# Kernel tuning notes

Hardware: AMD Instinct MI355X
Metric: run time of the kernel (lower is better)

## Reference

```python
import jax, jax.numpy as jnp
import numpy as np

N_LAYER = 4
N_HEAD = 12
D_MODEL = 768
SEQ_LEN = 2048
VOCAB = 50257
BATCH = 2


def _sinusoid_pe(seq_len, d_model):
    pos = np.arange(seq_len, dtype=np.float32)[:, None]
    div = np.exp(np.arange(0, d_model, 2, dtype=np.float32) * (-np.log(10000.0) / d_model))
    pe = np.zeros((seq_len, d_model), dtype=np.float32)
    pe[:, 0::2] = np.sin(pos * div)
    pe[:, 1::2] = np.cos(pos * div)
    return jnp.asarray(pe[None])  # [1, C, D]


def setup_inputs() -> dict:
    key = jax.random.key(0)
    ks = jax.random.split(key, 12)
    s = 0.02
    return {
        "features": jax.random.randint(ks[0], (BATCH, SEQ_LEN), 0, VOCAB),
        "targets": jax.random.randint(ks[1], (BATCH, SEQ_LEN), 0, VOCAB),
        "tok_embed": jax.random.normal(ks[2], (VOCAB, D_MODEL), jnp.float32) * s,
        "pos_emb": _sinusoid_pe(SEQ_LEN, D_MODEL),
        "ln1_w": jnp.ones((N_LAYER, D_MODEL), jnp.float32),
        "ln1_b": jnp.zeros((N_LAYER, D_MODEL), jnp.float32),
        "attn_w": jax.random.normal(ks[3], (N_LAYER, D_MODEL, 3 * D_MODEL), jnp.float32) * s,
        "attn_b": jnp.zeros((N_LAYER, 3 * D_MODEL), jnp.float32),
        "proj_w": jax.random.normal(ks[4], (N_LAYER, D_MODEL, D_MODEL), jnp.float32) * s,
        "proj_b": jnp.zeros((N_LAYER, D_MODEL), jnp.float32),
        "ln2_w": jnp.ones((N_LAYER, D_MODEL), jnp.float32),
        "ln2_b": jnp.zeros((N_LAYER, D_MODEL), jnp.float32),
        "ffn_w1": jax.random.normal(ks[5], (N_LAYER, D_MODEL, 4 * D_MODEL), jnp.float32) * s,
        "ffn_b1": jnp.zeros((N_LAYER, 4 * D_MODEL), jnp.float32),
        "ffn_w2": jax.random.normal(ks[6], (N_LAYER, 4 * D_MODEL, D_MODEL), jnp.float32) * s,
        "ffn_b2": jnp.zeros((N_LAYER, D_MODEL), jnp.float32),
        "lnf_w": jnp.ones((D_MODEL,), jnp.float32),
        "lnf_b": jnp.zeros((D_MODEL,), jnp.float32),
        "final_w": jax.random.normal(ks[7], (D_MODEL, VOCAB), jnp.float32) * s,
    }


def _layernorm(x, w, b, eps=1e-5):
    mu = jnp.mean(x, axis=-1, keepdims=True)
    var = jnp.var(x, axis=-1, keepdims=True)
    return (x - mu) * jax.lax.rsqrt(var + eps) * w + b


def _attention(x, wqkv, bqkv, wo, bo):
    B, C, E = x.shape
    dh = E // N_HEAD
    qkv = x @ wqkv + bqkv  # [B, C, 3E]
    q, k, v = jnp.split(qkv, 3, axis=-1)
    q = q.reshape(B, C, N_HEAD, dh)
    k = k.reshape(B, C, N_HEAD, dh)
    v = v.reshape(B, C, N_HEAD, dh)
    att = jnp.einsum("bqhd,bkhd->bhqk", q, k) / jnp.sqrt(jnp.float32(dh))
    causal = jnp.tril(jnp.ones((C, C), bool))
    att = jnp.where(causal, att, -jnp.inf)
    att = jax.nn.softmax(att, axis=-1)
    y = jnp.einsum("bhqk,bkhd->bqhd", att, v).reshape(B, C, E)
    return y @ wo + bo


def reference(features, targets, tok_embed, pos_emb, ln1_w, ln1_b, attn_w, attn_b,
              proj_w, proj_b, ln2_w, ln2_b, ffn_w1, ffn_b1, ffn_w2, ffn_b2,
              lnf_w, lnf_b, final_w):
    C = features.shape[1]
    x = tok_embed[features] + pos_emb[:, :C]
    for l in range(N_LAYER):
        h = _layernorm(x, ln1_w[l], ln1_b[l])
        x = x + _attention(h, attn_w[l], attn_b[l], proj_w[l], proj_b[l])
        h = _layernorm(x, ln2_w[l], ln2_b[l])
        h = jax.nn.gelu(h @ ffn_w1[l] + ffn_b1[l], approximate=False) @ ffn_w2[l] + ffn_b2[l]
        x = x + h
    x = _layernorm(x, lnf_w, lnf_b)
    logits = x @ final_w  # [B, C, V]
    logp = jax.nn.log_softmax(logits, axis=-1)
    tgt = targets.reshape(-1)
    valid = tgt != -1
    tgt_safe = jnp.where(valid, tgt, 0)
    nll = -jnp.take_along_axis(logp.reshape(-1, logits.shape[-1]), tgt_safe[:, None], axis=1)[:, 0]
    loss = jnp.sum(jnp.where(valid, nll, 0.0)) / jnp.maximum(jnp.sum(valid), 1)
    return logits, loss
```

## Files before the change

kernel.cpp:

```cpp
#include <hip/hip_runtime.h>
#include <math.h>

#define N_LAYER 4
#define N_HEAD  12
#define D_MODEL 768
#define SEQ     2048
#define VOCAB   50257
#define BATCH   2
#define MROWS   (BATCH*SEQ)

typedef __bf16 bf16;
typedef __bf16 bf16x8 __attribute__((ext_vector_type(8)));
typedef float  f32x4  __attribute__((ext_vector_type(4)));
typedef short  short8v __attribute__((ext_vector_type(8)));

__device__ __forceinline__ void gload16(const bf16* g, const bf16* l) {
    __builtin_amdgcn_global_load_lds(
        (const __attribute__((address_space(1))) void*)g,
        (__attribute__((address_space(3))) void*)l,
        16, 0, 0);
}

__global__ __launch_bounds__(256) void embed_kernel(
    const int* __restrict__ feat, const float* __restrict__ tok,
    const float* __restrict__ pos, float* __restrict__ x)
{
    int row = blockIdx.x;
    int cpos = row & (SEQ - 1);
    int tid = feat[row];
    const float* te = tok + (size_t)tid * D_MODEL;
    const float* pe = pos + (size_t)cpos * D_MODEL;
    float* xr = x + (size_t)row * D_MODEL;
    for (int c = threadIdx.x; c < D_MODEL; c += 256)
        xr[c] = te[c] + pe[c];
}

__global__ __launch_bounds__(256) void ln_kernel(
    const float* __restrict__ x, const float* __restrict__ w,
    const float* __restrict__ b, bf16* __restrict__ out)
{
    int row = blockIdx.x;
    const float* xr = x + (size_t)row * D_MODEL;
    float lv[3];
    float s = 0.f, ss = 0.f;
#pragma unroll
    for (int i = 0; i < 3; i++) {
        float v = xr[threadIdx.x + i * 256];
        lv[i] = v; s += v; ss += v * v;
    }
#pragma unroll
    for (int o = 32; o; o >>= 1) { s += __shfl_down(s, o, 64); ss += __shfl_down(ss, o, 64); }
    __shared__ float red[8];
    int wid = threadIdx.x >> 6;
    if ((threadIdx.x & 63) == 0) { red[wid] = s; red[wid + 4] = ss; }
    __syncthreads();
    s  = red[0] + red[1] + red[2] + red[3];
    ss = red[4] + red[5] + red[6] + red[7];
    float mu  = s * (1.f / D_MODEL);
    float var = ss * (1.f / D_MODEL) - mu * mu;
    float rs  = rsqrtf(var + 1e-5f);
#pragma unroll
    for (int i = 0; i < 3; i++) {
        int c = threadIdx.x + i * 256;
        out[(size_t)row * D_MODEL + c] = (bf16)((lv[i] - mu) * rs * w[c] + b[c]);
    }
}

__global__ __launch_bounds__(256) void transpose_conv_kernel(
    const float* __restrict__ W, bf16* __restrict__ Wt, int K, int N)
{
    int l = blockIdx.z;
    const float* Wl = W + (size_t)l * K * N;
    bf16* Wtl = Wt + (size_t)l * K * N;
    __shared__ float tile[32][33];
    int k0 = blockIdx.y * 32, n0 = blockIdx.x * 32;
    for (int idx = threadIdx.x; idx < 1024; idx += 256) {
        int i = idx >> 5, j = idx & 31;
        int n = n0 + j;
        tile[i][j] = (n < N) ? Wl[(size_t)(k0 + i) * N + n] : 0.f;
    }
    __syncthreads();
    for (int idx = threadIdx.x; idx < 1024; idx += 256) {
        int j = idx >> 5, i = idx & 31;
        int n = n0 + j;
        if (n < N) Wtl[(size_t)n * K + k0 + i] = (bf16)tile[i][j];
    }
}

__global__ __launch_bounds__(256) void vtrans_kernel(
    const bf16* __restrict__ qkv, bf16* __restrict__ vT)
{
    int j0 = blockIdx.x * 64, h = blockIdx.y, b = blockIdx.z;
    __shared__ bf16 t[64][72];
    const bf16* src = qkv + ((size_t)b * SEQ + j0) * (3 * D_MODEL) + 2 * D_MODEL + h * 64;
    int tid = threadIdx.x;
#pragma unroll
    for (int i = 0; i < 2; i++) {
        int c = tid + i * 256;
        int j = c >> 3, d8 = (c & 7) * 8;
        *(short8v*)&t[j][d8] = *(const short8v*)&src[(size_t)j * (3 * D_MODEL) + d8];
    }
    __syncthreads();
    bf16* dst = vT + ((size_t)(b * N_HEAD + h) * 64) * SEQ;
#pragma unroll
    for (int i = 0; i < 2; i++) {
        int c = tid + i * 256;
        int d = c >> 3, j8 = (c & 7) * 8;
        bf16 tmp[8];
#pragma unroll
        for (int e = 0; e < 8; e++) tmp[e] = t[j8 + e][d];
        *(short8v*)&dst[(size_t)d * SEQ + j0 + j8] = *(const short8v*)tmp;
    }
}

template<bool BIAS, bool GELU_, int OUTM, bool SWZ, bool LSE>
__global__ __launch_bounds__(256) void gemm_kernel(
    const bf16* __restrict__ A, const bf16* __restrict__ Bt,
    const float* __restrict__ bias, void* __restrict__ Cout,
    float* __restrict__ rowsum,
    int M, int N, int K)
{
    __shared__ __align__(16) bf16 As[128 * 32];
    __shared__ __align__(16) bf16 Bs[128 * 32];
    int tid = threadIdx.x;
    int lane = tid & 63, wid = tid >> 6;

    int nbx = gridDim.x;
    int bid = blockIdx.y * nbx + blockIdx.x;
    if (SWZ) {
        int nwg = nbx * gridDim.y;
        int q = nwg >> 3, r = nwg & 7;
        int xcd = bid & 7, loc = bid >> 3;
        bid = (xcd < r ? xcd * (q + 1) : r * (q + 1) + (xcd - r) * q) + loc;
    }
    int row0 = (bid % nbx) * 128;
    int col0 = (bid / nbx) * 128;

    int wr = (wid >> 1) * 64, wc = (wid & 1) * 64;

    int srow = wid * 16 + (lane >> 2);
    int selem = (lane & 3) * 8;
    const bf16* Ab0 = A + (size_t)(row0 + srow) * K + selem;
    const bf16* Ab1 = Ab0 + (size_t)64 * K;
    int bn0 = col0 + srow;      if (bn0 >= N) bn0 = N - 1;
    int bn1 = col0 + srow + 64; if (bn1 >= N) bn1 = N - 1;
    const bf16* Bb0 = Bt + (size_t)bn0 * K + selem;
    const bf16* Bb1 = Bt + (size_t)bn1 * K + selem;
    bf16* ldsA0 = As + wid * 512;
    bf16* ldsA1 = As + (wid + 4) * 512;
    bf16* ldsB0 = Bs + wid * 512;
    bf16* ldsB1 = Bs + (wid + 4) * 512;

    f32x4 acc[4][4] = {};
    int fr = lane & 15, fg8 = (lane >> 4) * 8;

    for (int k0 = 0; k0 < K; k0 += 32) {
        if (k0) __syncthreads();
        gload16(Ab0 + k0, ldsA0);
        gload16(Ab1 + k0, ldsA1);
        gload16(Bb0 + k0, ldsB0);
        gload16(Bb1 + k0, ldsB1);
        __syncthreads();

        bf16x8 af[4], bfr[4];
#pragma unroll
        for (int m = 0; m < 4; m++) af[m] = *(const bf16x8*)&As[(wr + m * 16 + fr) * 32 + fg8];
#pragma unroll
        for (int n = 0; n < 4; n++) bfr[n] = *(const bf16x8*)&Bs[(wc + n * 16 + fr) * 32 + fg8];
#pragma unroll
        for (int m = 0; m < 4; m++)
#pragma unroll
            for (int n = 0; n < 4; n++)
                acc[m][n] = __builtin_amdgcn_mfma_f32_16x16x32_bf16(af[m], bfr[n], acc[m][n], 0, 0, 0);
    }

    int g = lane >> 4;
    float lsum[4][4];
#pragma unroll
    for (int m = 0; m < 4; m++)
#pragma unroll
        for (int r = 0; r < 4; r++) lsum[m][r] = 0.f;

#pragma unroll
    for (int m = 0; m < 4; m++) {
#pragma unroll
        for (int n = 0; n < 4; n++) {
            int col = col0 + wc + n * 16 + fr;
            bool ok = (col < N);
            float bv = (BIAS && ok) ? bias[col] : 0.f;
#pragma unroll
            for (int r = 0; r < 4; r++) {
                int row = row0 + wr + m * 16 + g * 4 + r;
                float v = acc[m][n][r] + bv;
                if (GELU_) v = 0.5f * v * (1.f + erff(v * 0.70710678118f));
                if (ok) {
                    if (OUTM == 0)      ((float*)Cout)[(size_t)row * N + col] = v;
                    else if (OUTM == 1) ((bf16*)Cout)[(size_t)row * N + col] = (bf16)v;
                    else                ((float*)Cout)[(size_t)row * N + col] += v;
                }
                if (LSE) lsum[m][r] += ok ? __expf(v) : 0.f;
            }
        }
    }

    if (LSE) {
#pragma unroll
        for (int m = 0; m < 4; m++)
#pragma unroll
            for (int r = 0; r < 4; r++) {
                float s = lsum[m][r];
#pragma unroll
                for (int o = 1; o < 16; o <<= 1) s += __shfl_xor(s, o, 64);
                lsum[m][r] = s;
            }
        if (fr == 0) {
#pragma unroll
            for (int m = 0; m < 4; m++)
#pragma unroll
                for (int r = 0; r < 4; r++)
                    atomicAdd(&rowsum[row0 + wr + m * 16 + g * 4 + r], lsum[m][r]);
        }
    }
}

__global__ __launch_bounds__(256) void attn_kernel(
    const bf16* __restrict__ qkv, const bf16* __restrict__ vT, bf16* __restrict__ y)
{
    int qt = blockIdx.x, h = blockIdx.y, b = blockIdx.z;
    const size_t rs = 3 * D_MODEL;
    int tid = threadIdx.x, lane = tid & 63, wid = tid >> 6;
    int fr = lane & 15, g = lane >> 4;
    int wq = qt * 64 + wid * 16;

    const bf16* qb = qkv + (size_t)b * SEQ * rs + h * 64;
    const bf16* kb = qb + D_MODEL;
    const bf16* vb = vT + ((size_t)(b * N_HEAD + h) * 64) * SEQ;

    __shared__ bf16 Ps[4][16][72];

    bf16x8 aq[2];
#pragma unroll
    for (int kk = 0; kk < 2; kk++)
        aq[kk] = *(const bf16x8*)&qb[(size_t)(wq + fr) * rs + kk * 32 + g * 8];

    f32x4 acco[4] = {};
    float mrow[4], lrow[4];
#pragma unroll
    for (int r = 0; r < 4; r++) { mrow[r] = -1e30f; lrow[r] = 0.f; }

    int jmax = qt * 64;
    for (int j0 = 0; j0 <= jmax; j0 += 64) {
        f32x4 accs[4] = {};
#pragma unroll
        for (int n = 0; n < 4; n++)
#pragma unroll
            for (int kk = 0; kk < 2; kk++) {
                bf16x8 bk = *(const bf16x8*)&kb[(size_t)(j0 + n * 16 + fr) * rs + kk * 32 + g * 8];
                accs[n] = __builtin_amdgcn_mfma_f32_16x16x32_bf16(aq[kk], bk, accs[n], 0, 0, 0);
            }

        bool diag = (j0 == jmax);
#pragma unroll
        for (int n = 0; n < 4; n++) {
            int jc = j0 + n * 16 + fr;
#pragma unroll
            for (int r = 0; r < 4; r++) {
                float sv = accs[n][r] * 0.125f;
                if (diag) { int irow = wq + g * 4 + r; if (jc > irow) sv = -1e30f; }
                accs[n][r] = sv;
            }
        }

        float pscale[4];
#pragma unroll
        for (int r = 0; r < 4; r++) {
            float pm = fmaxf(fmaxf(accs[0][r], accs[1][r]), fmaxf(accs[2][r], accs[3][r]));
#pragma unroll
            for (int o = 1; o < 16; o <<= 1) pm = fmaxf(pm, __shfl_xor(pm, o, 64));
            float mnew = fmaxf(mrow[r], pm);
            float corr = __expf(mrow[r] - mnew);
            mrow[r] = mnew;
            float ls = 0.f;
#pragma unroll
            for (int n = 0; n < 4; n++) {
                float p = __expf(accs[n][r] - mnew);
                accs[n][r] = p; ls += p;
            }
#pragma unroll
            for (int o = 1; o < 16; o <<= 1) ls += __shfl_xor(ls, o, 64);
            lrow[r] = lrow[r] * corr + ls;
            pscale[r] = corr;
        }
#pragma unroll
        for (int n = 0; n < 4; n++)
#pragma unroll
            for (int r = 0; r < 4; r++) acco[n][r] *= pscale[r];

#pragma unroll
        for (int n = 0; n < 4; n++)
#pragma unroll
            for (int r = 0; r < 4; r++)
                Ps[wid][g * 4 + r][n * 16 + fr] = (bf16)accs[n][r];

        bf16x8 ap[2];
#pragma unroll
        for (int kk = 0; kk < 2; kk++)
            ap[kk] = *(const bf16x8*)&Ps[wid][fr][kk * 32 + g * 8];
#pragma unroll
        for (int kk = 0; kk < 2; kk++)
#pragma unroll
            for (int n = 0; n < 4; n++) {
                bf16x8 bv = *(const bf16x8*)&vb[(size_t)(n * 16 + fr) * SEQ + j0 + kk * 32 + g * 8];
                acco[n] = __builtin_amdgcn_mfma_f32_16x16x32_bf16(ap[kk], bv, acco[n], 0, 0, 0);
            }
    }

    bf16* yb = y + (size_t)b * SEQ * D_MODEL + h * 64;
#pragma unroll
    for (int n = 0; n < 4; n++)
#pragma unroll
        for (int r = 0; r < 4; r++) {
            int row = wq + g * 4 + r;
            yb[(size_t)row * D_MODEL + n * 16 + fr] = (bf16)(acco[n][r] / lrow[r]);
        }
}

__global__ __launch_bounds__(256) void loss_nll_kernel(
    const float* __restrict__ logits, const float* __restrict__ rowsum,
    const int* __restrict__ tgt, float* __restrict__ accum)
{
    int row = blockIdx.x * 256 + threadIdx.x;
    if (row >= MROWS) return;
    int t = tgt[row];
    if (t >= 0) {
        float nll = logf(rowsum[row]) - logits[(size_t)row * VOCAB + t];
        atomicAdd(accum, nll);
        atomicAdd(accum + 1, 1.f);
    }
}

__global__ void loss_final_kernel(const float* __restrict__ accum, float* __restrict__ out)
{
    out[0] = accum[0] / fmaxf(accum[1], 1.f);
}

extern "C" void kernel_launch(void* const* d_in, const int* in_sizes, int n_in,
                              void* d_out, int out_size, void* d_ws, size_t ws_size,
                              hipStream_t stream)
{
    const int*   feat  = (const int*)d_in[0];
    const int*   tgt   = (const int*)d_in[1];
    const float* tok   = (const float*)d_in[2];
    const float* pos   = (const float*)d_in[3];
    const float* ln1w  = (const float*)d_in[4];
    const float* ln1b  = (const float*)d_in[5];
    const float* attnw = (const float*)d_in[6];
    const float* attnb = (const float*)d_in[7];
    const float* projw = (const float*)d_in[8];
    const float* projb = (const float*)d_in[9];
    const float* ln2w  = (const float*)d_in[10];
    const float* ln2b  = (const float*)d_in[11];
    const float* fw1   = (const float*)d_in[12];
    const float* fb1   = (const float*)d_in[13];
    const float* fw2   = (const float*)d_in[14];
    const float* fb2   = (const float*)d_in[15];
    const float* lnfw  = (const float*)d_in[16];
    const float* lnfb  = (const float*)d_in[17];
    const float* finw  = (const float*)d_in[18];

    char* ws = (char*)d_ws;
    size_t off = 0;
    auto alloc = [&](size_t bytes) -> void* {
        void* p = ws + off; off += (bytes + 255) & ~(size_t)255; return p;
    };
    float* x     = (float*)alloc((size_t)MROWS * D_MODEL * 4);
    bf16*  h     = (bf16*) alloc((size_t)MROWS * D_MODEL * 2);
    bf16*  big   = (bf16*) alloc((size_t)MROWS * 4 * D_MODEL * 2);
    bf16*  ybuf  = (bf16*) alloc((size_t)MROWS * D_MODEL * 2);
    bf16*  vT    = (bf16*) alloc((size_t)BATCH * N_HEAD * 64 * SEQ * 2);
    bf16*  awt   = (bf16*) alloc((size_t)N_LAYER * 3 * D_MODEL * D_MODEL * 2);
    bf16*  pwt   = (bf16*) alloc((size_t)N_LAYER * D_MODEL * D_MODEL * 2);
    bf16*  f1wt  = (bf16*) alloc((size_t)N_LAYER * 4 * D_MODEL * D_MODEL * 2);
    bf16*  f2wt  = (bf16*) alloc((size_t)N_LAYER * 4 * D_MODEL * D_MODEL * 2);
    bf16*  fwt   = (bf16*) alloc((size_t)VOCAB * D_MODEL * 2);
    float* rowsum= (float*)alloc((size_t)MROWS * 4);
    float* accum = (float*)alloc(256);

    float* logits = (float*)d_out;
    float* lossp  = (float*)d_out + (size_t)MROWS * VOCAB;

    dim3 blk(256);
    transpose_conv_kernel<<<dim3(3 * D_MODEL / 32, D_MODEL / 32, N_LAYER), blk, 0, stream>>>(attnw, awt, D_MODEL, 3 * D_MODEL);
    transpose_conv_kernel<<<dim3(D_MODEL / 32, D_MODEL / 32, N_LAYER), blk, 0, stream>>>(projw, pwt, D_MODEL, D_MODEL);
    transpose_conv_kernel<<<dim3(4 * D_MODEL / 32, D_MODEL / 32, N_LAYER), blk, 0, stream>>>(fw1, f1wt, D_MODEL, 4 * D_MODEL);
    transpose_conv_kernel<<<dim3(D_MODEL / 32, 4 * D_MODEL / 32, N_LAYER), blk, 0, stream>>>(fw2, f2wt, 4 * D_MODEL, D_MODEL);
    transpose_conv_kernel<<<dim3((VOCAB + 31) / 32, D_MODEL / 32, 1), blk, 0, stream>>>(finw, fwt, D_MODEL, VOCAB);

    embed_kernel<<<MROWS, blk, 0, stream>>>(feat, tok, pos, x);

    for (int l = 0; l < N_LAYER; l++) {
        ln_kernel<<<MROWS, blk, 0, stream>>>(x, ln1w + l * D_MODEL, ln1b + l * D_MODEL, h);
        gemm_kernel<true, false, 1, false, false><<<dim3(MROWS / 128, (3 * D_MODEL) / 128), blk, 0, stream>>>(
            h, awt + (size_t)l * 3 * D_MODEL * D_MODEL, attnb + l * 3 * D_MODEL, big, nullptr,
            MROWS, 3 * D_MODEL, D_MODEL);
        vtrans_kernel<<<dim3(SEQ / 64, N_HEAD, BATCH), blk, 0, stream>>>(big, vT);
        attn_kernel<<<dim3(SEQ / 64, N_HEAD, BATCH), blk, 0, stream>>>(big, vT, ybuf);
        gemm_kernel<true, false, 2, false, false><<<dim3(MROWS / 128, D_MODEL / 128), blk, 0, stream>>>(
            ybuf, pwt + (size_t)l * D_MODEL * D_MODEL, projb + l * D_MODEL, x, nullptr,
            MROWS, D_MODEL, D_MODEL);
        ln_kernel<<<MROWS, blk, 0, stream>>>(x, ln2w + l * D_MODEL, ln2b + l * D_MODEL, h);
        gemm_kernel<true, true, 1, false, false><<<dim3(MROWS / 128, (4 * D_MODEL) / 128), blk, 0, stream>>>(
            h, f1wt + (size_t)l * 4 * D_MODEL * D_MODEL, fb1 + l * 4 * D_MODEL, big, nullptr,
            MROWS, 4 * D_MODEL, D_MODEL);
        gemm_kernel<true, false, 2, false, false><<<dim3(MROWS / 128, D_MODEL / 128), blk, 0, stream>>>(
            big, f2wt + (size_t)l * 4 * D_MODEL * D_MODEL, fb2 + l * D_MODEL, x, nullptr,
            MROWS, D_MODEL, 4 * D_MODEL);
    }

    ln_kernel<<<MROWS, blk, 0, stream>>>(x, lnfw, lnfb, h);

    hipMemsetAsync(rowsum, 0, (size_t)MROWS * 4, stream);
    hipMemsetAsync(accum, 0, 8, stream);

    gemm_kernel<false, false, 0, true, true><<<dim3(MROWS / 128, (VOCAB + 127) / 128), blk, 0, stream>>>(
        h, fwt, nullptr, logits, rowsum, MROWS, VOCAB, D_MODEL);

    loss_nll_kernel<<<(MROWS + 255) / 256, blk, 0, stream>>>(logits, rowsum, tgt, accum);
    loss_final_kernel<<<1, 1, 0, stream>>>(accum, lossp);

    (void)in_sizes; (void)n_in; (void)out_size; (void)ws_size;
}
```

Before: 2.274 ms.

## Split-K the residual projection GEMMs with atomic accumulation; nontemporal logits stores

Adds a SPLITK template parameter so the attention-output and FFN-down projections (N=768, only 192 blocks) launch two K-slices per tile and accumulate into the residual with atomicAdd, with bias added only by the first slice. This targets under-occupancy of the GPU on these small-N GEMMs. The logits GEMM now writes its fp32 output with nontemporal stores to reduce cache pollution from the very large logits write. Atomics add traffic and make the summation order nondeterministic.

```diff
diff --git a/kernel.cpp b/kernel.cpp
--- a/kernel.cpp
+++ b/kernel.cpp
@@ -113,7 +113,7 @@
     }
 }
 
-template<bool BIAS, bool GELU_, int OUTM, bool SWZ, bool LSE>
+template<bool BIAS, bool GELU_, int OUTM, bool SWZ, bool LSE, int SPLITK>
 __global__ __launch_bounds__(256) void gemm_kernel(
     const bf16* __restrict__ A, const bf16* __restrict__ Bt,
     const float* __restrict__ bias, void* __restrict__ Cout,
@@ -124,6 +124,9 @@
     __shared__ __align__(16) bf16 Bs[128 * 32];
     int tid = threadIdx.x;
     int lane = tid & 63, wid = tid >> 6;
+
+    int Kslice = K / SPLITK;
+    int kbase = (SPLITK > 1) ? (int)blockIdx.z * Kslice : 0;
 
     int nbx = gridDim.x;
     int bid = blockIdx.y * nbx + blockIdx.x;
@@ -140,12 +143,12 @@
 
     int srow = wid * 16 + (lane >> 2);
     int selem = (lane & 3) * 8;
-    const bf16* Ab0 = A + (size_t)(row0 + srow) * K + selem;
+    const bf16* Ab0 = A + (size_t)(row0 + srow) * K + kbase + selem;
     const bf16* Ab1 = Ab0 + (size_t)64 * K;
     int bn0 = col0 + srow;      if (bn0 >= N) bn0 = N - 1;
     int bn1 = col0 + srow + 64; if (bn1 >= N) bn1 = N - 1;
-    const bf16* Bb0 = Bt + (size_t)bn0 * K + selem;
-    const bf16* Bb1 = Bt + (size_t)bn1 * K + selem;
+    const bf16* Bb0 = Bt + (size_t)bn0 * K + kbase + selem;
+    const bf16* Bb1 = Bt + (size_t)bn1 * K + kbase + selem;
     bf16* ldsA0 = As + wid * 512;
     bf16* ldsA1 = As + (wid + 4) * 512;
     bf16* ldsB0 = Bs + wid * 512;
@@ -154,7 +157,7 @@
     f32x4 acc[4][4] = {};
     int fr = lane & 15, fg8 = (lane >> 4) * 8;
 
-    for (int k0 = 0; k0 < K; k0 += 32) {
+    for (int k0 = 0; k0 < Kslice; k0 += 32) {
         if (k0) __syncthreads();
         gload16(Ab0 + k0, ldsA0);
         gload16(Ab1 + k0, ldsA1);
@@ -175,6 +178,7 @@
     }
 
     int g = lane >> 4;
+    bool addbias = BIAS && (SPLITK == 1 || blockIdx.z == 0);
     float lsum[4][4];
 #pragma unroll
     for (int m = 0; m < 4; m++)
@@ -187,16 +191,21 @@
         for (int n = 0; n < 4; n++) {
             int col = col0 + wc + n * 16 + fr;
             bool ok = (col < N);
-            float bv = (BIAS && ok) ? bias[col] : 0.f;
+            float bv = (addbias && ok) ? bias[col] : 0.f;
 #pragma unroll
             for (int r = 0; r < 4; r++) {
                 int row = row0 + wr + m * 16 + g * 4 + r;
                 float v = acc[m][n][r] + bv;
                 if (GELU_) v = 0.5f * v * (1.f + erff(v * 0.70710678118f));
                 if (ok) {
-                    if (OUTM == 0)      ((float*)Cout)[(size_t)row * N + col] = v;
-                    else if (OUTM == 1) ((bf16*)Cout)[(size_t)row * N + col] = (bf16)v;
-                    else                ((float*)Cout)[(size_t)row * N + col] += v;
+                    if (OUTM == 0)
+                        __builtin_nontemporal_store(v, &((float*)Cout)[(size_t)row * N + col]);
+                    else if (OUTM == 1)
+                        ((bf16*)Cout)[(size_t)row * N + col] = (bf16)v;
+                    else if (SPLITK > 1)
+                        atomicAdd(&((float*)Cout)[(size_t)row * N + col], v);
+                    else
+                        ((float*)Cout)[(size_t)row * N + col] += v;
                 }
                 if (LSE) lsum[m][r] += ok ? __expf(v) : 0.f;
             }
@@ -400,19 +409,19 @@
 
     for (int l = 0; l < N_LAYER; l++) {
         ln_kernel<<<MROWS, blk, 0, stream>>>(x, ln1w + l * D_MODEL, ln1b + l * D_MODEL, h);
-        gemm_kernel<true, false, 1, false, false><<<dim3(MROWS / 128, (3 * D_MODEL) / 128), blk, 0, stream>>>(
+        gemm_kernel<true, false, 1, false, false, 1><<<dim3(MROWS / 128, (3 * D_MODEL) / 128), blk, 0, stream>>>(
             h, awt + (size_t)l * 3 * D_MODEL * D_MODEL, attnb + l * 3 * D_MODEL, big, nullptr,
             MROWS, 3 * D_MODEL, D_MODEL);
         vtrans_kernel<<<dim3(SEQ / 64, N_HEAD, BATCH), blk, 0, stream>>>(big, vT);
         attn_kernel<<<dim3(SEQ / 64, N_HEAD, BATCH), blk, 0, stream>>>(big, vT, ybuf);
-        gemm_kernel<true, false, 2, false, false><<<dim3(MROWS / 128, D_MODEL / 128), blk, 0, stream>>>(
+        gemm_kernel<true, false, 2, false, false, 2><<<dim3(MROWS / 128, D_MODEL / 128, 2), blk, 0, stream>>>(
             ybuf, pwt + (size_t)l * D_MODEL * D_MODEL, projb + l * D_MODEL, x, nullptr,
             MROWS, D_MODEL, D_MODEL);
         ln_kernel<<<MROWS, blk, 0, stream>>>(x, ln2w + l * D_MODEL, ln2b + l * D_MODEL, h);
-        gemm_kernel<true, true, 1, false, false><<<dim3(MROWS / 128, (4 * D_MODEL) / 128), blk, 0, stream>>>(
+        gemm_kernel<true, true, 1, false, false, 1><<<dim3(MROWS / 128, (4 * D_MODEL) / 128), blk, 0, stream>>>(
             h, f1wt + (size_t)l * 4 * D_MODEL * D_MODEL, fb1 + l * 4 * D_MODEL, big, nullptr,
             MROWS, 4 * D_MODEL, D_MODEL);
-        gemm_kernel<true, false, 2, false, false><<<dim3(MROWS / 128, D_MODEL / 128), blk, 0, stream>>>(
+        gemm_kernel<true, false, 2, false, false, 2><<<dim3(MROWS / 128, D_MODEL / 128, 2), blk, 0, stream>>>(
             big, f2wt + (size_t)l * 4 * D_MODEL * D_MODEL, fb2 + l * D_MODEL, x, nullptr,
             MROWS, D_MODEL, 4 * D_MODEL);
     }
@@ -422,7 +431,7 @@
     hipMemsetAsync(rowsum, 0, (size_t)MROWS * 4, stream);
     hipMemsetAsync(accum, 0, 8, stream);
 
-    gemm_kernel<false, false, 0, true, true><<<dim3(MROWS / 128, (VOCAB + 127) / 128), blk, 0, stream>>>(
+    gemm_kernel<false, false, 0, true, true, 1><<<dim3(MROWS / 128, (VOCAB + 127) / 128), blk, 0, stream>>>(
         h, fwt, nullptr, logits, rowsum, MROWS, VOCAB, D_MODEL);
 
     loss_nll_kernel<<<(MROWS + 255) / 256, blk, 0, stream>>>(logits, rowsum, tgt, accum);
```

New measurement: 2.440 ms. 1.07x slower.
